# Optimization experiments

Hardware: AMD Instinct MI355X
Metric: run time of the kernel (lower is better)

Reference implementation:

```python
import jax, jax.numpy as jnp
import numpy as np

B, T, V, C, L, H = 2, 1024, 50257, 768, 12, 12
HD = C // H


def setup_inputs() -> dict:
    key = jax.random.key(0)
    ks = jax.random.split(key, 10)
    s = 0.02
    rn = lambda k, shp: (jax.random.normal(k, shp, jnp.float32) * s)
    return dict(
        idx=jax.random.randint(ks[0], (B, T), 0, V),
        wte=rn(ks[1], (V, C)),
        wpe=rn(ks[2], (T, C)),
        ln1_w=jnp.ones((L, C)), ln1_b=jnp.zeros((L, C)),
        attn_w=rn(ks[3], (L, C, 3 * C)), attn_b=jnp.zeros((L, 3 * C)),
        proj_w=rn(ks[4], (L, C, C)), proj_b=jnp.zeros((L, C)),
        ln2_w=jnp.ones((L, C)), ln2_b=jnp.zeros((L, C)),
        fc_w=rn(ks[5], (L, C, 4 * C)), fc_b=jnp.zeros((L, 4 * C)),
        fc2_w=rn(ks[6], (L, 4 * C, C)), fc2_b=jnp.zeros((L, C)),
        lnf_w=jnp.ones((C,)), lnf_b=jnp.zeros((C,)),
        lm_head_w=rn(ks[7], (V, C)),  # torch Linear layout [out, in]
    )


def _layer_norm(x, w, b):
    m = jnp.mean(x, axis=-1, keepdims=True)
    v = jnp.mean(jnp.square(x - m), axis=-1, keepdims=True)
    return (x - m) * jax.lax.rsqrt(v + 1e-5) * w + b


def reference(idx, wte, wpe, ln1_w, ln1_b, attn_w, attn_b, proj_w, proj_b,
              ln2_w, ln2_b, fc_w, fc_b, fc2_w, fc2_b, lnf_w, lnf_b, lm_head_w):
    x = wte[idx] + wpe[jnp.arange(T)]  # [B,T,C]
    mask = jnp.tril(jnp.ones((T, T), bool))

    def block(x, p):
        l1w, l1b, aw, ab, pw, pb, l2w, l2b, fw, fb, f2w, f2b = p
        h = _layer_norm(x, l1w, l1b)
        qkv = h @ aw + ab  # [B,T,3C]
        q, k, v = jnp.split(qkv, 3, axis=-1)
        split_heads = lambda t: t.reshape(B, T, H, HD).transpose(0, 2, 1, 3)
        q, k, v = split_heads(q), split_heads(k), split_heads(v)
        att = jnp.einsum('bhqd,bhkd->bhqk', q, k) * (1.0 / np.sqrt(HD))
        att = jnp.where(mask, att, -jnp.inf)
        att = jax.nn.softmax(att, axis=-1)
        y = jnp.einsum('bhqk,bhkd->bhqd', att, v)
        y = y.transpose(0, 2, 1, 3).reshape(B, T, C)
        x = x + y @ pw + pb
        h2 = _layer_norm(x, l2w, l2b)
        x = x + jax.nn.gelu(h2 @ fw + fb, approximate=True) @ f2w + f2b
        return x, None

    layer_params = (ln1_w, ln1_b, attn_w, attn_b, proj_w, proj_b,
                    ln2_w, ln2_b, fc_w, fc_b, fc2_w, fc2_b)
    x, _ = jax.lax.scan(block, x, layer_params)
    x = _layer_norm(x, lnf_w, lnf_b)
    logits = x @ lm_head_w.T  # [B,T,V]
    return logits
```

## Files before the change

### kernel.cpp

```cpp
#include <hip/hip_runtime.h>
#include <hip/hip_bf16.h>

#define Bsz 2
#define Tsz 1024
#define Vsz 50257
#define Csz 768
#define Lsz 12
#define Hsz 12
#define Msz 2048
#define VPAD 50304

typedef __attribute__((ext_vector_type(8))) short short8;
typedef __attribute__((ext_vector_type(4))) float f32x4;

__device__ __forceinline__ ushort f2bf(float f) {
  union { float f; unsigned u; } v; v.f = f;
  return (ushort)((v.u + 0x7FFFu + ((v.u >> 16) & 1u)) >> 16);
}

__device__ __forceinline__ void load_lds16(const void* g, void* l) {
  __builtin_amdgcn_global_load_lds(
      (const __attribute__((address_space(1))) unsigned int*)g,
      (__attribute__((address_space(3))) unsigned int*)l, 16, 0, 0);
}

__global__ void k_embed(const int* __restrict__ idx, const float* __restrict__ wte,
                        const float* __restrict__ wpe, float* __restrict__ x) {
  int m = blockIdx.x;
  int t = m & (Tsz - 1);
  const float* src = wte + (size_t)idx[m] * Csz;
  const float* pe  = wpe + (size_t)t * Csz;
  float* dst = x + (size_t)m * Csz;
  for (int c = threadIdx.x; c < Csz; c += 256)
    dst[c] = src[c] + pe[c];
}

__global__ void k_ln(const float* __restrict__ x, const float* __restrict__ w,
                     const float* __restrict__ b, ushort* __restrict__ out) {
  int r = blockIdx.x * 4 + (threadIdx.x >> 6);
  int lane = threadIdx.x & 63;
  const float* row = x + (size_t)r * Csz;
  float v[12];
  float s = 0.f, q = 0.f;
#pragma unroll
  for (int j = 0; j < 12; j++) {
    v[j] = row[lane + j * 64];
    s += v[j];
    q += v[j] * v[j];
  }
#pragma unroll
  for (int o = 1; o < 64; o <<= 1) {
    s += __shfl_xor(s, o, 64);
    q += __shfl_xor(q, o, 64);
  }
  float mean = s * (1.0f / Csz);
  float rstd = rsqrtf(q * (1.0f / Csz) - mean * mean + 1e-5f);
  ushort* o = out + (size_t)r * Csz;
#pragma unroll
  for (int j = 0; j < 12; j++) {
    int c = lane + j * 64;
    o[c] = f2bf((v[j] - mean) * rstd * w[c] + b[c]);
  }
}

__global__ void k_prep(const float* __restrict__ aw, const float* __restrict__ pw,
                       const float* __restrict__ fw, const float* __restrict__ f2w,
                       ushort* __restrict__ wT, int l0, size_t lstride) {
  int t = blockIdx.x;
  int ly = l0 + blockIdx.y;
  const float* src; int R, Cn; size_t doff;
  if (t < 1728)      { src = aw  + (size_t)ly * Csz * 3 * Csz; R = Csz;     Cn = 3 * Csz; doff = 0; }
  else if (t < 2304) { t -= 1728; src = pw  + (size_t)ly * Csz * Csz;     R = Csz;     Cn = Csz;     doff = (size_t)3 * Csz * Csz; }
  else if (t < 4608) { t -= 2304; src = fw  + (size_t)ly * Csz * 4 * Csz; R = Csz;     Cn = 4 * Csz; doff = (size_t)4 * Csz * Csz; }
  else               { t -= 4608; src = f2w + (size_t)ly * 4 * Csz * Csz; R = 4 * Csz; Cn = Csz;     doff = (size_t)8 * Csz * Csz; }
  ushort* dst = wT + (size_t)blockIdx.y * lstride + doff;

  __shared__ float tb[32][33];
  int ncx = Cn / 32;
  int c0 = (t % ncx) * 32, r0 = (t / ncx) * 32;
  int tx = threadIdx.x & 31, ty = threadIdx.x >> 5;
#pragma unroll
  for (int k = 0; k < 4; k++)
    tb[ty + 8 * k][tx] = src[(size_t)(r0 + ty + 8 * k) * Cn + c0 + tx];
  __syncthreads();
#pragma unroll
  for (int k = 0; k < 4; k++)
    dst[(size_t)(c0 + ty + 8 * k) * R + r0 + tx] = f2bf(tb[tx][ty + 8 * k]);
}

__global__ void k_f32_to_bf16_pad(const float* __restrict__ src, ushort* __restrict__ dst,
                                  int n_src, int n_tot) {
  int stride = gridDim.x * 256 * 4;
  for (int i = (blockIdx.x * 256 + threadIdx.x) * 4; i < n_tot; i += stride) {
    ushort4 o;
    if (i + 3 < n_src) {
      float4 v = *(const float4*)(src + i);
      o.x = f2bf(v.x); o.y = f2bf(v.y); o.z = f2bf(v.z); o.w = f2bf(v.w);
    } else {
      o.x = o.y = o.z = o.w = 0;
    }
    *(ushort4*)(dst + i) = o;
  }
}

template <int BM, int BN, int FM, int FN, int BK, int OUT, bool SWZ, int EPI, bool PIPE, int MINW>
__global__ __launch_bounds__(256, MINW) void k_gemm(
    const ushort* __restrict__ A, const ushort* __restrict__ Bt,
    const float* __restrict__ bias, const float* res,
    void* __restrict__ outv, int N, int K, int ntm) {
  constexpr int RPC = (BK == 64) ? 8 : 16;
  constexpr int NCHA = BM / RPC, NCH = (BM + BN) / RPC, CPW = NCH / 4;
  static_assert(NCH % 4 == 0, "chunk count must be divisible by wave count");
  constexpr int NBUF = PIPE ? 2 : 1;
  constexpr int STB = NBUF * (BM + BN) * BK * 2;
  constexpr int EPB = EPI ? (4 * 16 * 68 * 4) : 0;
  constexpr int SMB = STB > EPB ? STB : EPB;
  __shared__ __align__(16) char smem[SMB];

  int bid = blockIdx.x;
  if (SWZ) {
    int nwg = gridDim.x;
    bid = (bid & 7) * (nwg >> 3) + (bid >> 3);
  }
  int by = bid % ntm, bx = bid / ntm;
  int m0 = by * BM, n0 = bx * BN;

  int tid = threadIdx.x;
  int wid = tid >> 6, lane = tid & 63, lg = lane >> 4, lr = lane & 15;
  int wm = (wid >> 1) * (FM * 16), wn = (wid & 1) * (FN * 16);

  const f32x4 FZ = {0.f, 0.f, 0.f, 0.f};
  f32x4 acc[FM][FN];
#pragma unroll
  for (int i = 0; i < FM; i++)
#pragma unroll
    for (int j = 0; j < FN; j++) acc[i][j] = FZ;

  int srow, scol;
  if (BK == 64) { srow = lane >> 3; scol = ((lane & 7) ^ (srow & 7)) * 8; }
  else          { srow = lane >> 2; scol = ((lane & 3) ^ ((lane >> 3) & 3)) * 8; }

  const ushort* p[CPW];
  int ldso[CPW];
#pragma unroll
  for (int i = 0; i < CPW; i++) {
    int c = wid * CPW + i;
    ldso[i] = c * 512;
    if (c < NCHA) p[i] = A + (size_t)(m0 + c * RPC + srow) * K + scol;
    else          p[i] = Bt + (size_t)(n0 + (c - NCHA) * RPC + srow) * K + scol;
  }

  auto STAGE = [&](int buf) {
    ushort* Sb = (ushort*)smem + buf * (BM + BN) * BK;
#pragma unroll
    for (int i = 0; i < CPW; i++) {
      load_lds16(p[i], Sb + ldso[i]);
      p[i] += BK;
    }
  };
  auto COMPUTE = [&](int buf) {
    const ushort* Sb = (const ushort*)smem + buf * (BM + BN) * BK;
#pragma unroll
    for (int kk = 0; kk < BK / 32; kk++) {
      int cofs;
      if (BK == 64) cofs = (kk * 32 + lg * 8) ^ ((lr & 7) << 3);
      else          cofs = (lg * 8) ^ (((lr >> 1) & 3) << 3);
      short8 a[FM], b[FN];
#pragma unroll
      for (int f = 0; f < FM; f++)
        a[f] = *(const short8*)&Sb[(wm + f * 16 + lr) * BK + cofs];
#pragma unroll
      for (int f = 0; f < FN; f++)
        b[f] = *(const short8*)&Sb[(BM + wn + f * 16 + lr) * BK + cofs];
#pragma unroll
      for (int fi = 0; fi < FM; fi++)
#pragma unroll
        for (int fj = 0; fj < FN; fj++)
          acc[fi][fj] = __builtin_amdgcn_mfma_f32_16x16x32_bf16(a[fi], b[fj], acc[fi][fj], 0, 0, 0);
    }
  };

  if (PIPE) {
    int NT = K / BK;
    STAGE(0);
    __syncthreads();
    for (int t = 0;;) {
      if (t + 1 < NT) STAGE(1);
      COMPUTE(0);
      if (++t == NT) break;
      __syncthreads();
      if (t + 1 < NT) STAGE(0);
      COMPUTE(1);
      if (++t == NT) break;
      __syncthreads();
    }
  } else {
    int NT = K / BK;
    for (int t = 0; t < NT; t++) {
      STAGE(0);
      __syncthreads();
      COMPUTE(0);
      __syncthreads();
    }
  }

  if constexpr (EPI) {
    __syncthreads();
    float* Sf = (float*)smem + wid * (16 * 68);
#pragma unroll
    for (int fi = 0; fi < FM; fi++) {
#pragma unroll
      for (int fj = 0; fj < 4; fj++)
#pragma unroll
        for (int i = 0; i < 4; i++)
          Sf[(4 * lg + i) * 68 + fj * 16 + lr] = acc[fi][fj][i];
#pragma unroll
      for (int it = 0; it < 4; it++) {
        int rl = it * 4 + lg;
        f32x4 v = *(const f32x4*)&Sf[rl * 68 + lr * 4];
        int gm = m0 + wm + fi * 16 + rl;
        int gn = n0 + wn + lr * 4;
        float* op = (float*)outv + (size_t)gm * N + gn;
        if (gn + 3 < N) {
          *(f32x4*)op = v;
        } else {
#pragma unroll
          for (int j = 0; j < 4; j++)
            if (gn + j < N) op[j] = v[j];
        }
      }
    }
    return;
  }

#pragma unroll
  for (int fi = 0; fi < FM; fi++)
#pragma unroll
    for (int fj = 0; fj < FN; fj++) {
      int gn = n0 + wn + fj * 16 + lr;
      if (gn < N) {
        float bv = bias ? bias[gn] : 0.f;
#pragma unroll
        for (int i = 0; i < 4; i++) {
          int gm = m0 + wm + fi * 16 + 4 * lg + i;
          size_t o = (size_t)gm * N + gn;
          float v = acc[fi][fj][i] + bv;
          if (OUT == 0) {
            if (res) v += res[o];
            ((float*)outv)[o] = v;
          } else if (OUT == 1) {
            ((ushort*)outv)[o] = f2bf(v);
          } else if (OUT == 3) {
            if (gn < Csz) v *= 0.18033688f;
            ((ushort*)outv)[o] = f2bf(v);
          } else {
            float u = 0.7978845608f * (v + 0.044715f * v * v * v);
            float t2 = __expf(2.f * u);
            float th = 1.f - 2.f / (t2 + 1.f);
            ((ushort*)outv)[o] = f2bf(0.5f * v * (1.f + th));
          }
        }
      }
    }
}

__global__ __launch_bounds__(256) void k_attn(const ushort* __restrict__ qkv,
                                              ushort* __restrict__ ybf) {
  __shared__ __align__(16) ushort Ks[128 * 72];
  __shared__ __align__(16) ushort Vs[64 * 136];
  __shared__ __align__(16) ushort Ps[4 * 16 * 136];
  int bid = blockIdx.x;
  bid = (bid & 7) * ((Bsz * Hsz * 16) >> 3) + (bid >> 3);
  int bh = bid >> 4;
  int q0 = (15 - (bid & 15)) * 64;
  int b = bh / Hsz, h = bh % Hsz;
  int tid = threadIdx.x, wid = tid >> 6, lane = tid & 63, lg = lane >> 4, lr = lane & 15;
  const ushort* base = qkv + (size_t)b * Tsz * 2304;

  int qt = q0 + wid * 16 + lr;
  const ushort* qp = base + (size_t)qt * 2304 + h * 64;
  short8 aq0 = *(const short8*)(qp + lg * 8);
  short8 aq1 = *(const short8*)(qp + 32 + lg * 8);

  int srow = tid >> 3, soff = (tid & 7) * 8;
  const ushort* kp0 = base + (size_t)srow * 2304 + 768 + h * 64 + soff;
  const ushort* vp0 = kp0 + 768;
  short8 kreg[4], vreg[4];
  auto LOADKV = [&](int k0) {
#pragma unroll
    for (int r = 0; r < 4; r++) {
      kreg[r] = *(const short8*)(kp0 + (size_t)(k0 + r * 32) * 2304);
      vreg[r] = *(const short8*)(vp0 + (size_t)(k0 + r * 32) * 2304);
    }
  };
  auto WRITEKV = [&]() {
#pragma unroll
    for (int r = 0; r < 4; r++) {
      int row = srow + r * 32;
      *(short8*)&Ks[row * 72 + soff] = kreg[r];
#pragma unroll
      for (int j = 0; j < 8; j++) Vs[(soff + j) * 136 + row] = (ushort)vreg[r][j];
    }
  };

  const f32x4 FZ = {0.f, 0.f, 0.f, 0.f};
  f32x4 of[4];
  of[0] = FZ; of[1] = FZ; of[2] = FZ; of[3] = FZ;
  float lrow[4] = {0.f, 0.f, 0.f, 0.f};

  int nkt = (q0 >> 7) + 1;
  LOADKV(0);
  for (int kt = 0; kt < nkt; kt++) {
    int k0 = kt * 128;
    WRITEKV();
    __syncthreads();
    if (kt + 1 < nkt) LOADKV(k0 + 128);

    f32x4 sf[8];
#pragma unroll
    for (int nf = 0; nf < 8; nf++) {
      sf[nf] = FZ;
      short8 b0 = *(const short8*)&Ks[(nf * 16 + lr) * 72 + lg * 8];
      short8 b1 = *(const short8*)&Ks[(nf * 16 + lr) * 72 + 32 + lg * 8];
      sf[nf] = __builtin_amdgcn_mfma_f32_16x16x32_bf16(aq0, b0, sf[nf], 0, 0, 0);
      sf[nf] = __builtin_amdgcn_mfma_f32_16x16x32_bf16(aq1, b1, sf[nf], 0, 0, 0);
    }

    bool last = (kt == nkt - 1);
#pragma unroll
    for (int i = 0; i < 4; i++) {
      int qr = q0 + wid * 16 + 4 * lg + i;
      float rs = 0.f;
#pragma unroll
      for (int nf = 0; nf < 8; nf++) {
        float s = sf[nf][i];
        if (last && k0 + nf * 16 + lr > qr) s = -INFINITY;
        float pv = exp2f(s);
        rs += pv;
        Ps[(wid * 16 + 4 * lg + i) * 136 + nf * 16 + lr] = f2bf(pv);
      }
#pragma unroll
      for (int o = 1; o < 16; o <<= 1) rs += __shfl_xor(rs, o, 16);
      lrow[i] += rs;
    }

    short8 ap[4];
#pragma unroll
    for (int c = 0; c < 4; c++)
      ap[c] = *(const short8*)&Ps[(wid * 16 + lr) * 136 + c * 32 + lg * 8];
#pragma unroll
    for (int df = 0; df < 4; df++) {
#pragma unroll
      for (int c = 0; c < 4; c++) {
        short8 bv = *(const short8*)&Vs[(df * 16 + lr) * 136 + c * 32 + lg * 8];
        of[df] = __builtin_amdgcn_mfma_f32_16x16x32_bf16(ap[c], bv, of[df], 0, 0, 0);
      }
    }
    __syncthreads();
  }

  ushort* yp = ybf + (size_t)b * Tsz * Csz;
#pragma unroll
  for (int df = 0; df < 4; df++)
#pragma unroll
    for (int i = 0; i < 4; i++) {
      int qr = q0 + wid * 16 + 4 * lg + i;
      float v = of[df][i] / lrow[i];
      yp[(size_t)qr * Csz + h * 64 + df * 16 + lr] = f2bf(v);
    }
}

extern "C" void kernel_launch(void* const* d_in, const int* in_sizes, int n_in,
                              void* d_out, int out_size, void* d_ws, size_t ws_size,
                              hipStream_t stream) {
  (void)in_sizes; (void)n_in; (void)out_size;
  const int* idx      = (const int*)d_in[0];
  const float* wte    = (const float*)d_in[1];
  const float* wpe    = (const float*)d_in[2];
  const float* ln1_w  = (const float*)d_in[3];
  const float* ln1_b  = (const float*)d_in[4];
  const float* attn_w = (const float*)d_in[5];
  const float* attn_b = (const float*)d_in[6];
  const float* proj_w = (const float*)d_in[7];
  const float* proj_b = (const float*)d_in[8];
  const float* ln2_w  = (const float*)d_in[9];
  const float* ln2_b  = (const float*)d_in[10];
  const float* fc_w   = (const float*)d_in[11];
  const float* fc_b   = (const float*)d_in[12];
  const float* fc2_w  = (const float*)d_in[13];
  const float* fc2_b  = (const float*)d_in[14];
  const float* lnf_w  = (const float*)d_in[15];
  const float* lnf_b  = (const float*)d_in[16];
  const float* lm_w   = (const float*)d_in[17];
  float* out = (float*)d_out;

  char* ws = (char*)d_ws;
  float*  x     = (float*)(ws + 0);
  ushort* qkvbf = (ushort*)(ws + 6291456);
  ushort* abuf  = (ushort*)(ws + 15728640);
  ushort* hbuf  = (ushort*)(ws + 18874368);
  ushort* lmw   = (ushort*)(ws + 31457280);
  ushort* wT    = (ushort*)(ws + 108724224);
  const size_t LSTRIDE = (size_t)12 * Csz * Csz;
  const size_t NEED_FULL = 108724224ull + LSTRIDE * 2 * Lsz;
  bool full = ws_size >= NEED_FULL;

  k_embed<<<Msz, 256, 0, stream>>>(idx, wte, wpe, x);
  k_f32_to_bf16_pad<<<4096, 256, 0, stream>>>(lm_w, lmw, Vsz * Csz, VPAD * Csz);
  if (full)
    k_prep<<<dim3(6912, Lsz), 256, 0, stream>>>(attn_w, proj_w, fc_w, fc2_w, wT, 0, LSTRIDE);

  for (int l = 0; l < Lsz; l++) {
    ushort* wTl = wT + (full ? (size_t)l * LSTRIDE : 0);
    if (!full)
      k_prep<<<dim3(6912, 1), 256, 0, stream>>>(attn_w, proj_w, fc_w, fc2_w, wTl, l, 0);
    const ushort* qkvW = wTl;
    const ushort* projW = wTl + (size_t)3 * Csz * Csz;
    const ushort* fcW   = wTl + (size_t)4 * Csz * Csz;
    const ushort* fc2W  = wTl + (size_t)8 * Csz * Csz;

    k_ln<<<Msz / 4, 256, 0, stream>>>(x, ln1_w + l * Csz, ln1_b + l * Csz, abuf);
    k_gemm<128, 96, 4, 3, 64, 3, false, 0, true, 1><<<(Msz / 128) * (3 * Csz / 96), 256, 0, stream>>>(
        abuf, qkvW, attn_b + (size_t)l * 3 * Csz, nullptr, qkvbf, 3 * Csz, Csz, Msz / 128);
    k_attn<<<Bsz * Hsz * 16, 256, 0, stream>>>(qkvbf, abuf);
    k_gemm<64, 96, 2, 3, 64, 0, false, 0, true, 1><<<(Msz / 64) * (Csz / 96), 256, 0, stream>>>(
        abuf, projW, proj_b + (size_t)l * Csz, x, x, Csz, Csz, Msz / 64);
    k_ln<<<Msz / 4, 256, 0, stream>>>(x, ln2_w + l * Csz, ln2_b + l * Csz, abuf);
    k_gemm<128, 128, 4, 4, 64, 2, false, 0, true, 1><<<(Msz / 128) * (4 * Csz / 128), 256, 0, stream>>>(
        abuf, fcW, fc_b + (size_t)l * 4 * Csz, nullptr, hbuf, 4 * Csz, Csz, Msz / 128);
    k_gemm<64, 96, 2, 3, 64, 0, false, 0, true, 1><<<(Msz / 64) * (Csz / 96), 256, 0, stream>>>(
        hbuf, fc2W, fc2_b + (size_t)l * Csz, x, x, Csz, 4 * Csz, Msz / 64);
  }

  k_ln<<<Msz / 4, 256, 0, stream>>>(x, lnf_w, lnf_b, abuf);
  int ntm = Msz / 64;
  k_gemm<64, 128, 2, 4, 64, 0, true, 0, false, 1><<<ntm * (VPAD / 128), 256, 0, stream>>>(
      abuf, lmw, nullptr, nullptr, out, Vsz, Csz, ntm);
}
```

Before: 2.307 ms.

## Fuse layernorm into GEMM A-loads using row stats accumulated in residual epilogues

```diff
diff --git a/kernel.cpp b/kernel.cpp
--- a/kernel.cpp
+++ b/kernel.cpp
@@ -25,41 +25,30 @@
 }
 
 __global__ void k_embed(const int* __restrict__ idx, const float* __restrict__ wte,
-                        const float* __restrict__ wpe, float* __restrict__ x) {
+                        const float* __restrict__ wpe, float* __restrict__ x,
+                        float* __restrict__ st0) {
   int m = blockIdx.x;
   int t = m & (Tsz - 1);
   const float* src = wte + (size_t)idx[m] * Csz;
   const float* pe  = wpe + (size_t)t * Csz;
   float* dst = x + (size_t)m * Csz;
-  for (int c = threadIdx.x; c < Csz; c += 256)
-    dst[c] = src[c] + pe[c];
-}
-
-__global__ void k_ln(const float* __restrict__ x, const float* __restrict__ w,
-                     const float* __restrict__ b, ushort* __restrict__ out) {
-  int r = blockIdx.x * 4 + (threadIdx.x >> 6);
-  int lane = threadIdx.x & 63;
-  const float* row = x + (size_t)r * Csz;
-  float v[12];
-  float s = 0.f, q = 0.f;
-#pragma unroll
-  for (int j = 0; j < 12; j++) {
-    v[j] = row[lane + j * 64];
-    s += v[j];
-    q += v[j] * v[j];
-  }
-#pragma unroll
-  for (int o = 1; o < 64; o <<= 1) {
-    s += __shfl_xor(s, o, 64);
-    q += __shfl_xor(q, o, 64);
-  }
-  float mean = s * (1.0f / Csz);
-  float rstd = rsqrtf(q * (1.0f / Csz) - mean * mean + 1e-5f);
-  ushort* o = out + (size_t)r * Csz;
-#pragma unroll
-  for (int j = 0; j < 12; j++) {
-    int c = lane + j * 64;
-    o[c] = f2bf((v[j] - mean) * rstd * w[c] + b[c]);
+  int tid = threadIdx.x;
+  float v0 = src[tid] + pe[tid];
+  float v1 = src[tid + 256] + pe[tid + 256];
+  float v2 = src[tid + 512] + pe[tid + 512];
+  dst[tid] = v0; dst[tid + 256] = v1; dst[tid + 512] = v2;
+  float s = v0 + v1 + v2, q = v0 * v0 + v1 * v1 + v2 * v2;
+  for (int o = 32; o; o >>= 1) {
+    s += __shfl_down(s, o, 64);
+    q += __shfl_down(q, o, 64);
+  }
+  __shared__ float red[8];
+  int wid = tid >> 6, lane = tid & 63;
+  if (!lane) { red[wid] = s; red[4 + wid] = q; }
+  __syncthreads();
+  if (!tid) {
+    st0[m * 2]     = red[0] + red[1] + red[2] + red[3];
+    st0[m * 2 + 1] = red[4] + red[5] + red[6] + red[7];
   }
 }
 
@@ -103,19 +92,21 @@
   }
 }
 
-template <int BM, int BN, int FM, int FN, int BK, int OUT, bool SWZ, int EPI, bool PIPE, int MINW>
+template <int BM, int BN, int FM, int FN, int BK, int OUT, bool SWZ, bool PIPE, int MINW,
+          bool LNA, bool STATS>
 __global__ __launch_bounds__(256, MINW) void k_gemm(
     const ushort* __restrict__ A, const ushort* __restrict__ Bt,
     const float* __restrict__ bias, const float* res,
-    void* __restrict__ outv, int N, int K, int ntm) {
+    void* __restrict__ outv, int N, int K, int ntm,
+    const float* __restrict__ xln, const float* __restrict__ stin,
+    const float* __restrict__ lnw, const float* __restrict__ lnb,
+    float* __restrict__ stout) {
   constexpr int RPC = (BK == 64) ? 8 : 16;
   constexpr int NCHA = BM / RPC, NCH = (BM + BN) / RPC, CPW = NCH / 4;
   static_assert(NCH % 4 == 0, "chunk count must be divisible by wave count");
+  static_assert(!LNA || BK == 64, "LNA path implemented for BK=64 only");
   constexpr int NBUF = PIPE ? 2 : 1;
-  constexpr int STB = NBUF * (BM + BN) * BK * 2;
-  constexpr int EPB = EPI ? (4 * 16 * 68 * 4) : 0;
-  constexpr int SMB = STB > EPB ? STB : EPB;
-  __shared__ __align__(16) char smem[SMB];
+  __shared__ __align__(16) ushort smem[NBUF * (BM + BN) * BK];
 
   int bid = blockIdx.x;
   if (SWZ) {
@@ -146,20 +137,49 @@
   for (int i = 0; i < CPW; i++) {
     int c = wid * CPW + i;
     ldso[i] = c * 512;
-    if (c < NCHA) p[i] = A + (size_t)(m0 + c * RPC + srow) * K + scol;
-    else          p[i] = Bt + (size_t)(n0 + (c - NCHA) * RPC + srow) * K + scol;
-  }
-
-  auto STAGE = [&](int buf) {
-    ushort* Sb = (ushort*)smem + buf * (BM + BN) * BK;
+    if (c < NCHA) {
+      if (!LNA) p[i] = A + (size_t)(m0 + c * RPC + srow) * K + scol;
+      else      p[i] = nullptr;
+    } else {
+      p[i] = Bt + (size_t)(n0 + (c - NCHA) * RPC + srow) * K + scol;
+    }
+  }
+
+  auto STAGE = [&](int buf, int k0) {
+    ushort* Sb = smem + buf * (BM + BN) * BK;
 #pragma unroll
     for (int i = 0; i < CPW; i++) {
-      load_lds16(p[i], Sb + ldso[i]);
-      p[i] += BK;
+      int c = wid * CPW + i;
+      if (LNA && c < NCHA) {
+        int r = lane >> 3, ls = lane & 7;
+        int grow = m0 + c * 8 + r;
+        float sm = stin[grow * 2], s2 = stin[grow * 2 + 1];
+        float mean = sm * (1.f / Csz);
+        float rstd = rsqrtf(s2 * (1.f / Csz) - mean * mean + 1e-5f);
+        const float* xp = xln + (size_t)grow * Csz + k0 + ls * 8;
+        float4 x0 = *(const float4*)xp, x1 = *(const float4*)(xp + 4);
+        const float* wp = lnw + k0 + ls * 8;
+        const float* bp = lnb + k0 + ls * 8;
+        float4 w0 = *(const float4*)wp, w1 = *(const float4*)(wp + 4);
+        float4 b0 = *(const float4*)bp, b1 = *(const float4*)(bp + 4);
+        short8 pk;
+        pk[0] = (short)f2bf((x0.x - mean) * rstd * w0.x + b0.x);
+        pk[1] = (short)f2bf((x0.y - mean) * rstd * w0.y + b0.y);
+        pk[2] = (short)f2bf((x0.z - mean) * rstd * w0.z + b0.z);
+        pk[3] = (short)f2bf((x0.w - mean) * rstd * w0.w + b0.w);
+        pk[4] = (short)f2bf((x1.x - mean) * rstd * w1.x + b1.x);
+        pk[5] = (short)f2bf((x1.y - mean) * rstd * w1.y + b1.y);
+        pk[6] = (short)f2bf((x1.z - mean) * rstd * w1.z + b1.z);
+        pk[7] = (short)f2bf((x1.w - mean) * rstd * w1.w + b1.w);
+        *(short8*)&Sb[(c * 8 + r) * BK + ((ls ^ r) & 7) * 8] = pk;
+      } else {
+        load_lds16(p[i], Sb + ldso[i]);
+        p[i] += BK;
+      }
     }
   };
   auto COMPUTE = [&](int buf) {
-    const ushort* Sb = (const ushort*)smem + buf * (BM + BN) * BK;
+    const ushort* Sb = smem + buf * (BM + BN) * BK;
 #pragma unroll
     for (int kk = 0; kk < BK / 32; kk++) {
       int cofs;
@@ -180,57 +200,36 @@
     }
   };
 
+  int NT = K / BK;
   if (PIPE) {
-    int NT = K / BK;
-    STAGE(0);
+    int kn = BK;
+    STAGE(0, 0);
     __syncthreads();
     for (int t = 0;;) {
-      if (t + 1 < NT) STAGE(1);
+      if (t + 1 < NT) { STAGE(1, kn); kn += BK; }
       COMPUTE(0);
       if (++t == NT) break;
       __syncthreads();
-      if (t + 1 < NT) STAGE(0);
+      if (t + 1 < NT) { STAGE(0, kn); kn += BK; }
       COMPUTE(1);
       if (++t == NT) break;
       __syncthreads();
     }
   } else {
-    int NT = K / BK;
     for (int t = 0; t < NT; t++) {
-      STAGE(0);
+      STAGE(0, t * BK);
       __syncthreads();
       COMPUTE(0);
       __syncthreads();
     }
   }
 
-  if constexpr (EPI) {
-    __syncthreads();
-    float* Sf = (float*)smem + wid * (16 * 68);
-#pragma unroll
-    for (int fi = 0; fi < FM; fi++) {
-#pragma unroll
-      for (int fj = 0; fj < 4; fj++)
-#pragma unroll
-        for (int i = 0; i < 4; i++)
-          Sf[(4 * lg + i) * 68 + fj * 16 + lr] = acc[fi][fj][i];
-#pragma unroll
-      for (int it = 0; it < 4; it++) {
-        int rl = it * 4 + lg;
-        f32x4 v = *(const f32x4*)&Sf[rl * 68 + lr * 4];
-        int gm = m0 + wm + fi * 16 + rl;
-        int gn = n0 + wn + lr * 4;
-        float* op = (float*)outv + (size_t)gm * N + gn;
-        if (gn + 3 < N) {
-          *(f32x4*)op = v;
-        } else {
-#pragma unroll
-          for (int j = 0; j < 4; j++)
-            if (gn + j < N) op[j] = v[j];
-        }
-      }
-    }
-    return;
+  float ps[FM][4], pq[FM][4];
+  if (STATS) {
+#pragma unroll
+    for (int fi = 0; fi < FM; fi++)
+#pragma unroll
+      for (int i = 0; i < 4; i++) { ps[fi][i] = 0.f; pq[fi][i] = 0.f; }
   }
 
 #pragma unroll
@@ -247,6 +246,7 @@
           float v = acc[fi][fj][i] + bv;
           if (OUT == 0) {
             if (res) v += res[o];
+            if (STATS) { ps[fi][i] += v; pq[fi][i] += v * v; }
             ((float*)outv)[o] = v;
           } else if (OUT == 1) {
             ((ushort*)outv)[o] = f2bf(v);
@@ -262,6 +262,25 @@
         }
       }
     }
+
+  if (STATS) {
+#pragma unroll
+    for (int fi = 0; fi < FM; fi++)
+#pragma unroll
+      for (int i = 0; i < 4; i++) {
+        float a = ps[fi][i], b2 = pq[fi][i];
+#pragma unroll
+        for (int o = 1; o < 16; o <<= 1) {
+          a  += __shfl_xor(a, o, 16);
+          b2 += __shfl_xor(b2, o, 16);
+        }
+        if (lr == 0) {
+          int gm = m0 + wm + fi * 16 + 4 * lg + i;
+          atomicAdd(stout + gm * 2, a);
+          atomicAdd(stout + gm * 2 + 1, b2);
+        }
+      }
+  }
 }
 
 __global__ __launch_bounds__(256) void k_attn(const ushort* __restrict__ qkv,
@@ -399,13 +418,16 @@
   ushort* qkvbf = (ushort*)(ws + 6291456);
   ushort* abuf  = (ushort*)(ws + 15728640);
   ushort* hbuf  = (ushort*)(ws + 18874368);
-  ushort* lmw   = (ushort*)(ws + 31457280);
-  ushort* wT    = (ushort*)(ws + 108724224);
+  float*  stats = (float*)(ws + 31457280);
+  ushort* lmw   = (ushort*)(ws + 31866880);
+  ushort* wT    = (ushort*)(ws + 109133824);
   const size_t LSTRIDE = (size_t)12 * Csz * Csz;
-  const size_t NEED_FULL = 108724224ull + LSTRIDE * 2 * Lsz;
+  const size_t NEED_FULL = 109133824ull + LSTRIDE * 2 * Lsz;
   bool full = ws_size >= NEED_FULL;
-
-  k_embed<<<Msz, 256, 0, stream>>>(idx, wte, wpe, x);
+  const int STSL = 2048 * 2;
+
+  hipMemsetAsync(stats, 0, 25 * STSL * 4, stream);
+  k_embed<<<Msz, 256, 0, stream>>>(idx, wte, wpe, x, stats);
   k_f32_to_bf16_pad<<<4096, 256, 0, stream>>>(lm_w, lmw, Vsz * Csz, VPAD * Csz);
   if (full)
     k_prep<<<dim3(6912, Lsz), 256, 0, stream>>>(attn_w, proj_w, fc_w, fc2_w, wT, 0, LSTRIDE);
@@ -419,21 +441,28 @@
     const ushort* fcW   = wTl + (size_t)4 * Csz * Csz;
     const ushort* fc2W  = wTl + (size_t)8 * Csz * Csz;
 
-    k_ln<<<Msz / 4, 256, 0, stream>>>(x, ln1_w + l * Csz, ln1_b + l * Csz, abuf);
-    k_gemm<128, 96, 4, 3, 64, 3, false, 0, true, 1><<<(Msz / 128) * (3 * Csz / 96), 256, 0, stream>>>(
-        abuf, qkvW, attn_b + (size_t)l * 3 * Csz, nullptr, qkvbf, 3 * Csz, Csz, Msz / 128);
+    k_gemm<128, 96, 4, 3, 64, 3, false, true, 1, true, false>
+        <<<(Msz / 128) * (3 * Csz / 96), 256, 0, stream>>>(
+        nullptr, qkvW, attn_b + (size_t)l * 3 * Csz, nullptr, qkvbf, 3 * Csz, Csz, Msz / 128,
+        x, stats + (size_t)(2 * l) * STSL, ln1_w + l * Csz, ln1_b + l * Csz, nullptr);
     k_attn<<<Bsz * Hsz * 16, 256, 0, stream>>>(qkvbf, abuf);
-    k_gemm<64, 96, 2, 3, 64, 0, false, 0, true, 1><<<(Msz / 64) * (Csz / 96), 256, 0, stream>>>(
-        abuf, projW, proj_b + (size_t)l * Csz, x, x, Csz, Csz, Msz / 64);
-    k_ln<<<Msz / 4, 256, 0, stream>>>(x, ln2_w + l * Csz, ln2_b + l * Csz, abuf);
-    k_gemm<128, 128, 4, 4, 64, 2, false, 0, true, 1><<<(Msz / 128) * (4 * Csz / 128), 256, 0, stream>>>(
-        abuf, fcW, fc_b + (size_t)l * 4 * Csz, nullptr, hbuf, 4 * Csz, Csz, Msz / 128);
-    k_gemm<64, 96, 2, 3, 64, 0, false, 0, true, 1><<<(Msz / 64) * (Csz / 96), 256, 0, stream>>>(
-        hbuf, fc2W, fc2_b + (size_t)l * Csz, x, x, Csz, 4 * Csz, Msz / 64);
-  }
-
-  k_ln<<<Msz / 4, 256, 0, stream>>>(x, lnf_w, lnf_b, abuf);
+    k_gemm<64, 96, 2, 3, 64, 0, false, true, 1, false, true>
+        <<<(Msz / 64) * (Csz / 96), 256, 0, stream>>>(
+        abuf, projW, proj_b + (size_t)l * Csz, x, x, Csz, Csz, Msz / 64,
+        nullptr, nullptr, nullptr, nullptr, stats + (size_t)(2 * l + 1) * STSL);
+    k_gemm<128, 128, 4, 4, 64, 2, false, true, 1, true, false>
+        <<<(Msz / 128) * (4 * Csz / 128), 256, 0, stream>>>(
+        nullptr, fcW, fc_b + (size_t)l * 4 * Csz, nullptr, hbuf, 4 * Csz, Csz, Msz / 128,
+        x, stats + (size_t)(2 * l + 1) * STSL, ln2_w + l * Csz, ln2_b + l * Csz, nullptr);
+    k_gemm<64, 96, 2, 3, 64, 0, false, true, 1, false, true>
+        <<<(Msz / 64) * (Csz / 96), 256, 0, stream>>>(
+        hbuf, fc2W, fc2_b + (size_t)l * Csz, x, x, Csz, 4 * Csz, Msz / 64,
+        nullptr, nullptr, nullptr, nullptr, stats + (size_t)(2 * l + 2) * STSL);
+  }
+
   int ntm = Msz / 64;
-  k_gemm<64, 128, 2, 4, 64, 0, true, 0, false, 1><<<ntm * (VPAD / 128), 256, 0, stream>>>(
-      abuf, lmw, nullptr, nullptr, out, Vsz, Csz, ntm);
-}
+  k_gemm<64, 128, 2, 4, 64, 0, true, false, 1, true, false>
+      <<<ntm * (VPAD / 128), 256, 0, stream>>>(
+      nullptr, lmw, nullptr, nullptr, out, Vsz, Csz, ntm,
+      x, stats + (size_t)24 * STSL, lnf_w, lnf_b, nullptr);
+}
```

Result: slower. 4.081 ms (+76.9%).
